# Kernel tuning notes

Hardware: AMD Instinct MI355X
Metric: run time of the kernel (lower is better)

## Reference

```python
import jax, jax.numpy as jnp
import numpy as np

B, P, DIM, H, HKV = 4, 2048, 1024, 16, 8
D = DIM // H  # head_dim = 64


def setup_inputs() -> dict:
    key = jax.random.key(0)
    ks = jax.random.split(key, 5)
    s = lambda fan: 1.0 / np.sqrt(fan)
    return {
        "x": jax.random.normal(ks[0], (B, P, DIM), jnp.float32),
        "Wq": jax.random.normal(ks[1], (DIM, DIM), jnp.float32) * s(DIM),
        "Wk": jax.random.normal(ks[2], (DIM, HKV * D), jnp.float32) * s(DIM),
        "Wv": jax.random.normal(ks[3], (DIM, HKV * D), jnp.float32) * s(DIM),
        "Wp": jax.random.normal(ks[4], (DIM, DIM), jnp.float32) * s(DIM),
        "bp": jnp.zeros((DIM,), jnp.float32),
        "cache": jnp.zeros((HKV,), jnp.float32),  # registered buffer, starts at zero
    }


def _ratios(k, cache):
    # k: [B, HKV, P, D]; torch.norm over dims (2,3) then sum over batch -> [HKV]
    mags = jnp.sqrt((k * k).sum(axis=(2, 3))).sum(axis=0)
    diff = jnp.abs(cache - mags)
    r = jnp.round(diff / diff.sum() * H).astype(jnp.int32)
    # Deterministic repair of rounding so sum(r) == H (original uses random indices)
    r = jax.lax.while_loop(lambda r: r.sum() > H,
                           lambda r: r.at[jnp.argmax(r)].add(-1), r)
    r = jax.lax.while_loop(lambda r: r.sum() < H,
                           lambda r: r.at[jnp.argmin(r)].add(1), r)
    return r


def reference(x, Wq, Wk, Wv, Wp, bp, cache):
    # qkv projections (no bias, per qkv_bias=False)
    q = (x @ Wq).reshape(B, P, H, D).transpose(0, 2, 1, 3) * (D ** -0.5)  # [B,H,P,D]
    k = (x @ Wk).reshape(B, P, HKV, D).transpose(0, 2, 1, 3)              # [B,HKV,P,D]
    v = (x @ Wv).reshape(B, P, HKV, D).transpose(0, 2, 1, 3)

    # dynamic group sizes per kv head (inference path: cache <- magnitudes)
    ratios = jax.lax.stop_gradient(_ratios(k, cache))  # [HKV], sums to H
    # map each query head h to its kv head: group i owns heads [cumsum[i-1], cumsum[i])
    kv_id = jnp.searchsorted(jnp.cumsum(ratios), jnp.arange(H), side='right')

    # gather kv per query head -> identical math to the per-group loop, fully fused
    kf = k[:, kv_id]  # [B,H,P,D]
    vf = v[:, kv_id]
    scores = jnp.einsum('bhqd,bhkd->bhqk', q, kf)   # [B,H,P,P]
    w = jax.nn.softmax(scores, axis=-1)             # attn_drop p=0 -> identity
    out = jnp.einsum('bhqk,bhkd->bhqd', w, vf)
    out = out.transpose(0, 2, 1, 3).reshape(B, P, DIM)
    return out @ Wp + bp  # proj (proj_drop p=0)
```

## Files before the change

kernel.cpp:

```cpp
#include <hip/hip_runtime.h>

typedef __bf16 bf16x8 __attribute__((ext_vector_type(8)));
typedef __bf16 bf16x4 __attribute__((ext_vector_type(4)));
typedef float floatx4 __attribute__((ext_vector_type(4)));

#define BSZ 4
#define SEQ 2048
#define DIM 1024
#define NH 16
#define NKV 8
#define HD 64

#define QSCALE 0.18033688011112042f
#define CSHIFT -14.426950408889634f

#if __has_builtin(__builtin_amdgcn_exp2f)
#define EXP2(x) __builtin_amdgcn_exp2f(x)
#else
#define EXP2(x) exp2f(x)
#endif

#define GLDS16(g, l) __builtin_amdgcn_global_load_lds(                        \
    (const __attribute__((address_space(1))) void*)(g),                       \
    (__attribute__((address_space(3))) void*)(l), 16, 0, 0)

__global__ __launch_bounds__(256) void prep_kernel(
    const float* __restrict__ x,
    const float* __restrict__ Wq, const float* __restrict__ Wk,
    const float* __restrict__ Wv, const float* __restrict__ Wp,
    __bf16* __restrict__ xb, __bf16* __restrict__ Wt, __bf16* __restrict__ Wpt)
{
    __shared__ __bf16 T[64][72];
    const int bid = blockIdx.x;
    const int tid = threadIdx.x;

    if (bid < 2048) {
        size_t i = ((size_t)bid * 256 + tid) * 16;
#pragma unroll
        for (int q = 0; q < 2; ++q) {
            float4 a = *(const float4*)&x[i + q * 8];
            float4 b = *(const float4*)&x[i + q * 8 + 4];
            bf16x8 o;
            o[0] = (__bf16)a.x; o[1] = (__bf16)a.y; o[2] = (__bf16)a.z; o[3] = (__bf16)a.w;
            o[4] = (__bf16)b.x; o[5] = (__bf16)b.y; o[6] = (__bf16)b.z; o[7] = (__bf16)b.w;
            *(bf16x8*)&xb[i + q * 8] = o;
        }
        return;
    }

    const int t  = bid - 2048;
    const int k0 = (t & 15) * 64;
    const int cg = (t >> 4) * 64;

    const float* W; int ldn, cl, orow; __bf16* out;
    if (cg < 1024)      { W = Wq; ldn = 1024; cl = cg;        out = Wt;  orow = cg; }
    else if (cg < 1536) { W = Wk; ldn = 512;  cl = cg - 1024; out = Wt;  orow = cg; }
    else if (cg < 2048) { W = Wv; ldn = 512;  cl = cg - 1536; out = Wt;  orow = cg; }
    else                { W = Wp; ldn = 1024; cl = cg - 2048; out = Wpt; orow = cg - 2048; }

    const int kr = tid >> 2;
    const int cq = (tid & 3) * 16;
#pragma unroll
    for (int j = 0; j < 4; ++j) {
        float4 f = *(const float4*)&W[(size_t)(k0 + kr) * ldn + cl + cq + j * 4];
        T[cq + j * 4 + 0][kr] = (__bf16)f.x;
        T[cq + j * 4 + 1][kr] = (__bf16)f.y;
        T[cq + j * 4 + 2][kr] = (__bf16)f.z;
        T[cq + j * 4 + 3][kr] = (__bf16)f.w;
    }
    __syncthreads();
#pragma unroll
    for (int j = 0; j < 2; ++j) {
        int ch = tid * 2 + j;
        int c = ch >> 3, kc = (ch & 7) * 8;
        *(bf16x8*)&out[(size_t)(orow + c) * 1024 + k0 + kc] = *(bf16x8*)&T[c][kc];
    }
}

#define QSTAGE(bi, kk)                                                        \
    {                                                                         \
        GLDS16(Ag + (kk),             Asb + (bi) * 4096 + wv * 512);          \
        GLDS16(Ag + (kk) + 64 * 1024, Asb + (bi) * 4096 + 2048 + wv * 512);   \
        GLDS16(Bg + (kk),             Bsb + (bi) * 4096 + wv * 512);          \
        GLDS16(Bg + (kk) + 64 * 1024, Bsb + (bi) * 4096 + 2048 + wv * 512);   \
    }

__global__ __launch_bounds__(256) void qkv_gemm(
    const __bf16* __restrict__ xb, const __bf16* __restrict__ Wt,
    __bf16* __restrict__ qw, __bf16* __restrict__ kw, __bf16* __restrict__ vw)
{
    extern __shared__ __align__(16) __bf16 smem[];
    __bf16* Asb = smem;
    __bf16* Bsb = smem + 8192;

    const int m0 = blockIdx.y * 128;
    const int c0 = blockIdx.x * 128;

    const int tid  = threadIdx.x;
    const int lane = tid & 63, wv = tid >> 6;
    const int l16  = lane & 15, quad = lane >> 4;
    const int wr = (wv >> 1) * 64, wc = (wv & 1) * 64;

    const int srow = wv * 16 + (lane >> 2);
    const int skc  = (lane & 3) * 8;
    const __bf16* Ag = xb + (size_t)(m0 + srow) * 1024 + skc;
    const __bf16* Bg = Wt + (size_t)(c0 + srow) * 1024 + skc;

    floatx4 acc[4][4] = {};

    QSTAGE(0, 0);
    __syncthreads();

    for (int t = 0; t < 32; ++t) {
        const int cur = t & 1;
        if (t < 31) QSTAGE(cur ^ 1, (t + 1) * 32);

        bf16x8 af[4], bfr[4];
#pragma unroll
        for (int tt = 0; tt < 4; ++tt) {
            af[tt]  = *(bf16x8*)&Asb[cur * 4096 + (wr + tt * 16 + l16) * 32 + quad * 8];
            bfr[tt] = *(bf16x8*)&Bsb[cur * 4096 + (wc + tt * 16 + l16) * 32 + quad * 8];
        }
#pragma unroll
        for (int mt = 0; mt < 4; ++mt)
#pragma unroll
            for (int nt = 0; nt < 4; ++nt)
                acc[mt][nt] = __builtin_amdgcn_mfma_f32_16x16x32_bf16(
                    af[mt], bfr[nt], acc[mt][nt], 0, 0, 0);
        __syncthreads();
    }

    const int bb = m0 >> 11;
    if (c0 < 1536) {
#pragma unroll
        for (int mt = 0; mt < 4; ++mt) {
#pragma unroll
            for (int nt = 0; nt < 4; ++nt) {
#pragma unroll
                for (int r = 0; r < 4; ++r) {
                    int m = m0 + wr + mt * 16 + quad * 4 + r;
                    int c = c0 + wc + nt * 16 + l16;
                    int p = m & 2047;
                    float val = acc[mt][nt][r];
                    if (c < 1024) {
                        int h = c >> 6, d = c & 63;
                        qw[(((size_t)bb * NH + h) * SEQ + p) * HD + d] = (__bf16)(val * QSCALE);
                    } else {
                        int cc = c - 1024, hh = cc >> 6, d = cc & 63;
                        kw[(((size_t)bb * NKV + hh) * SEQ + p) * HD + d] = (__bf16)val;
                    }
                }
            }
        }
    } else {
        __bf16* T = smem;
#pragma unroll
        for (int mt = 0; mt < 4; ++mt)
#pragma unroll
            for (int nt = 0; nt < 4; ++nt) {
                bf16x4 pv;
#pragma unroll
                for (int r = 0; r < 4; ++r) pv[r] = (__bf16)acc[mt][nt][r];
                *(bf16x4*)&T[(wc + nt * 16 + l16) * 136 + wr + mt * 16 + quad * 4] = pv;
            }
        __syncthreads();

        const int c_l = tid >> 1, half = tid & 1;
        const int cc = c0 - 1536 + c_l, hh = cc >> 6, d = cc & 63;
        const int p0 = (m0 & 2047) + half * 64;
        __bf16* dst = &vw[((size_t)(bb * NKV + hh) * HD + d) * SEQ + p0];
        const __bf16* src = &T[c_l * 136 + half * 64];
#pragma unroll
        for (int i = 0; i < 8; ++i)
            *(bf16x8*)&dst[i * 8] = *(const bf16x8*)&src[i * 8];
    }
}

__global__ __launch_bounds__(256) void ksumsq(const __bf16* __restrict__ kw,
                                              float* __restrict__ partial)
{
    const int blk = blockIdx.x;
    const __bf16* base = kw + (size_t)(blk >> 3) * (SEQ * HD)
                            + (size_t)(blk & 7) * (SEQ * HD / 8);
    const int tid = threadIdx.x;

    float s = 0.f;
#pragma unroll
    for (int i = tid * 8; i < SEQ * HD / 8; i += 256 * 8) {
        bf16x8 vv = *(const bf16x8*)&base[i];
#pragma unroll
        for (int j = 0; j < 8; ++j) { float f = (float)vv[j]; s += f * f; }
    }
#pragma unroll
    for (int off = 1; off < 64; off <<= 1) s += __shfl_xor(s, off, 64);

    __shared__ float red[4];
    if ((tid & 63) == 0) red[tid >> 6] = s;
    __syncthreads();
    if (tid == 0) partial[blk] = red[0] + red[1] + red[2] + red[3];
}

__global__ void ratios_kernel(const float* __restrict__ partial,
                              const float* __restrict__ cache,
                              int* __restrict__ kv_id)
{
    if (threadIdx.x != 0 || blockIdx.x != 0) return;
    float mag[8] = {0.f, 0.f, 0.f, 0.f, 0.f, 0.f, 0.f, 0.f};
    for (int b = 0; b < 4; ++b)
        for (int j = 0; j < 8; ++j) {
            float ss = 0.f;
            for (int sl = 0; sl < 8; ++sl) ss += partial[(b * 8 + j) * 8 + sl];
            mag[j] += sqrtf(ss);
        }
    float diff[8], sum = 0.f;
    for (int j = 0; j < 8; ++j) {
        diff[j] = fabsf(cache[j] - mag[j]);
        sum += diff[j];
    }
    int r[8], s = 0;
    for (int j = 0; j < 8; ++j) {
        r[j] = (int)rintf(diff[j] / sum * 16.0f);
        s += r[j];
    }
    while (s > 16) {
        int jm = 0;
        for (int j = 1; j < 8; ++j) if (r[j] > r[jm]) jm = j;
        r[jm]--; s--;
    }
    while (s < 16) {
        int jm = 0;
        for (int j = 1; j < 8; ++j) if (r[j] < r[jm]) jm = j;
        r[jm]++; s++;
    }
    int cum[8], c = 0;
    for (int j = 0; j < 8; ++j) { c += r[j]; cum[j] = c; }
    for (int h = 0; h < 16; ++h) {
        int j = 0;
        while (j < 7 && cum[j] <= h) j++;
        kv_id[h] = j;
    }
}

__global__ __launch_bounds__(256, 2) void attn_kernel(
    const __bf16* __restrict__ qw, const __bf16* __restrict__ kw,
    const __bf16* __restrict__ vw, const int* __restrict__ kv_id,
    __bf16* __restrict__ attn_out)
{
    __shared__ __align__(16) __bf16 Kt[2][64 * 72];
    __shared__ __align__(16) __bf16 VT[2][64 * 72];

    const int bh = blockIdx.y;
    const int b = bh >> 4, h = bh & 15;
    const int q0 = blockIdx.x * 256;
    const int kv = kv_id[h];

    const __bf16* Kg = kw + ((size_t)(b * NKV + kv) * SEQ) * HD;
    const __bf16* Vg = vw + ((size_t)(b * NKV + kv) * HD) * SEQ;
    const __bf16* Qg = qw + ((size_t)(b * NH + h) * SEQ + q0) * HD;

    const int tid  = threadIdx.x;
    const int lane = tid & 63, wv = tid >> 6;
    const int l16  = lane & 15, quad = lane >> 4;

    bf16x8 qf[4][2];
#pragma unroll
    for (int s = 0; s < 4; ++s) {
        const __bf16* qp = &Qg[(size_t)(64 * wv + 16 * s + l16) * HD];
        qf[s][0] = *(const bf16x8*)&qp[quad * 8];
        qf[s][1] = *(const bf16x8*)&qp[32 + quad * 8];
    }

    bf16x8 vones;
#pragma unroll
    for (int j = 0; j < 8; ++j) vones[j] = (__bf16)1.0f;

    floatx4 o[4][4] = {};
    floatx4 ol[4] = {};

    const int row = tid >> 2, cc = (tid & 3) << 4;
    const __bf16* kp = Kg + (size_t)row * HD + cc;
    const __bf16* vp = Vg + (size_t)row * SEQ + cc;

    bf16x8 rk0 = *(const bf16x8*)kp;
    bf16x8 rk1 = *(const bf16x8*)(kp + 8);
    bf16x8 rv0 = *(const bf16x8*)vp;
    bf16x8 rv1 = *(const bf16x8*)(vp + 8);
    {
        __bf16* kd = &Kt[0][row * 72 + cc];
        *(bf16x8*)kd = rk0; *(bf16x8*)(kd + 8) = rk1;
        __bf16* vd = &VT[0][row * 72 + cc];
        *(bf16x8*)vd = rv0; *(bf16x8*)(vd + 8) = rv1;
    }
    __syncthreads();

    const floatx4 cinit = {CSHIFT, CSHIFT, CSHIFT, CSHIFT};

    for (int kb = 0; kb < 32; ++kb) {
        const int cur = kb & 1;
        const __bf16* Kc = &Kt[cur][0];
        const __bf16* Vc = &VT[cur][0];

        floatx4 sacc[4][4];
#pragma unroll
        for (int s = 0; s < 4; ++s)
#pragma unroll
            for (int t = 0; t < 4; ++t) sacc[s][t] = cinit;
        {
            bf16x8 kf[4];
#pragma unroll
            for (int t = 0; t < 4; ++t)
                kf[t] = *(bf16x8*)&Kc[(16 * t + l16) * 72 + quad * 8];
#pragma unroll
            for (int t = 0; t < 4; ++t)
#pragma unroll
                for (int s = 0; s < 4; ++s)
                    sacc[s][t] = __builtin_amdgcn_mfma_f32_16x16x32_bf16(
                        kf[t], qf[s][0], sacc[s][t], 0, 0, 0);
#pragma unroll
            for (int t = 0; t < 4; ++t)
                kf[t] = *(bf16x8*)&Kc[(16 * t + l16) * 72 + 32 + quad * 8];
#pragma unroll
            for (int t = 0; t < 4; ++t)
#pragma unroll
                for (int s = 0; s < 4; ++s)
                    sacc[s][t] = __builtin_amdgcn_mfma_f32_16x16x32_bf16(
                        kf[t], qf[s][1], sacc[s][t], 0, 0, 0);
        }

        if (kb < 31) {
            const __bf16* kn = kp + (size_t)(kb + 1) * (64 * HD);
            const __bf16* vn = vp + (kb + 1) * 64;
            rk0 = *(const bf16x8*)kn;
            rk1 = *(const bf16x8*)(kn + 8);
            rv0 = *(const bf16x8*)vn;
            rv1 = *(const bf16x8*)(vn + 8);
        }

        bf16x8 a0s[4], a1s[4];
#pragma unroll
        for (int s = 0; s < 4; ++s) {
            bf16x8 a0, a1;
#pragma unroll
            for (int r = 0; r < 4; ++r) {
                float e0 = EXP2(sacc[s][0][r]);
                float e1 = EXP2(sacc[s][1][r]);
                float e2 = EXP2(sacc[s][2][r]);
                float e3 = EXP2(sacc[s][3][r]);
                a0[r] = (__bf16)e0; a0[4 + r] = (__bf16)e1;
                a1[r] = (__bf16)e2; a1[4 + r] = (__bf16)e3;
            }
            a0s[s] = a0; a1s[s] = a1;
        }

#pragma unroll
        for (int s = 0; s < 4; ++s) {
            ol[s] = __builtin_amdgcn_mfma_f32_16x16x32_bf16(a0s[s], vones, ol[s], 0, 0, 0);
            ol[s] = __builtin_amdgcn_mfma_f32_16x16x32_bf16(a1s[s], vones, ol[s], 0, 0, 0);
        }

#pragma unroll
        for (int dt = 0; dt < 4; ++dt) {
            const __bf16* vrow = &Vc[(16 * dt + l16) * 72 + 4 * quad];
            bf16x4 lo0 = *(const bf16x4*)vrow;
            bf16x4 hi0 = *(const bf16x4*)(vrow + 16);
            bf16x8 vb0 = __builtin_shufflevector(lo0, hi0, 0, 1, 2, 3, 4, 5, 6, 7);
#pragma unroll
            for (int s = 0; s < 4; ++s)
                o[s][dt] = __builtin_amdgcn_mfma_f32_16x16x32_bf16(
                    a0s[s], vb0, o[s][dt], 0, 0, 0);
            bf16x4 lo1 = *(const bf16x4*)(vrow + 32);
            bf16x4 hi1 = *(const bf16x4*)(vrow + 48);
            bf16x8 vb1 = __builtin_shufflevector(lo1, hi1, 0, 1, 2, 3, 4, 5, 6, 7);
#pragma unroll
            for (int s = 0; s < 4; ++s)
                o[s][dt] = __builtin_amdgcn_mfma_f32_16x16x32_bf16(
                    a1s[s], vb1, o[s][dt], 0, 0, 0);
        }

        if (kb < 31) {
            __bf16* kd = &Kt[cur ^ 1][row * 72 + cc];
            *(bf16x8*)kd = rk0; *(bf16x8*)(kd + 8) = rk1;
            __bf16* vd = &VT[cur ^ 1][row * 72 + cc];
            *(bf16x8*)vd = rv0; *(bf16x8*)(vd + 8) = rv1;
        }
        __syncthreads();
    }

#pragma unroll
    for (int s = 0; s < 4; ++s) {
#pragma unroll
        for (int r = 0; r < 4; ++r) {
            float inv = 1.f / ol[s][r];
            int p_ = q0 + 64 * wv + 16 * s + quad * 4 + r;
#pragma unroll
            for (int dt = 0; dt < 4; ++dt) {
                int d = 16 * dt + l16;
                attn_out[(((size_t)b * SEQ + p_) * NH + h) * HD + d] = (__bf16)(o[s][dt][r] * inv);
            }
        }
    }
}

#define GSTAGE(bi, kk)                                                        \
    {                                                                         \
        GLDS16(Ag + (kk),             &As[bi][wv * 512]);                     \
        GLDS16(Ag + (kk) + 64 * 1024, &As[bi][2048 + wv * 512]);              \
        GLDS16(Bg + (kk),             &Bs[bi][wv * 512]);                     \
        GLDS16(Bg + (kk) + 64 * 1024, &Bs[bi][2048 + wv * 512]);              \
    }

__global__ __launch_bounds__(256) void proj_gemm(
    const __bf16* __restrict__ A, const __bf16* __restrict__ Wpt,
    const float* __restrict__ bp, float* __restrict__ out)
{
    __shared__ __align__(16) __bf16 As[2][128 * 32];
    __shared__ __align__(16) __bf16 Bs[2][128 * 32];

    const int m0 = blockIdx.y * 128, c0 = blockIdx.x * 128;
    const int tid = threadIdx.x, lane = tid & 63, wv = tid >> 6;
    const int l16 = lane & 15, quad = lane >> 4;
    const int wr = (wv >> 1) * 64, wc = (wv & 1) * 64;

    const int srow = wv * 16 + (lane >> 2);
    const int skc  = (lane & 3) * 8;
    const __bf16* Ag = A   + (size_t)(m0 + srow) * 1024 + skc;
    const __bf16* Bg = Wpt + (size_t)(c0 + srow) * 1024 + skc;

    floatx4 acc[4][4] = {};

    GSTAGE(0, 0);
    __syncthreads();

    for (int t = 0; t < 32; ++t) {
        const int cur = t & 1;
        if (t < 31) GSTAGE(cur ^ 1, (t + 1) * 32);

        bf16x8 af[4], bfr[4];
#pragma unroll
        for (int tt = 0; tt < 4; ++tt) {
            af[tt]  = *(bf16x8*)&As[cur][(wr + tt * 16 + l16) * 32 + quad * 8];
            bfr[tt] = *(bf16x8*)&Bs[cur][(wc + tt * 16 + l16) * 32 + quad * 8];
        }
#pragma unroll
        for (int mt = 0; mt < 4; ++mt)
#pragma unroll
            for (int nt = 0; nt < 4; ++nt)
                acc[mt][nt] = __builtin_amdgcn_mfma_f32_16x16x32_bf16(
                    af[mt], bfr[nt], acc[mt][nt], 0, 0, 0);
        __syncthreads();
    }

#pragma unroll
    for (int nt = 0; nt < 4; ++nt) {
        int c = c0 + wc + nt * 16 + l16;
        float bias = bp[c];
#pragma unroll
        for (int mt = 0; mt < 4; ++mt)
#pragma unroll
            for (int r = 0; r < 4; ++r) {
                int m = m0 + wr + mt * 16 + quad * 4 + r;
                out[(size_t)m * 1024 + c] = acc[mt][nt][r] + bias;
            }
    }
}

extern "C" void kernel_launch(void* const* d_in, const int* in_sizes, int n_in,
                              void* d_out, int out_size, void* d_ws, size_t ws_size,
                              hipStream_t stream)
{
    const float* x     = (const float*)d_in[0];
    const float* Wq    = (const float*)d_in[1];
    const float* Wk    = (const float*)d_in[2];
    const float* Wv    = (const float*)d_in[3];
    const float* Wp    = (const float*)d_in[4];
    const float* bp    = (const float*)d_in[5];
    const float* cache = (const float*)d_in[6];
    float* outp = (float*)d_out;

    __bf16* ws = (__bf16*)d_ws;
    __bf16* qw  = ws;
    __bf16* kw  = qw + (size_t)BSZ * NH * SEQ * HD;
    __bf16* vw  = kw + (size_t)BSZ * NKV * SEQ * HD;
    __bf16* at  = vw + (size_t)BSZ * NKV * SEQ * HD;
    __bf16* xb  = at + (size_t)BSZ * NH * SEQ * HD;
    __bf16* Wt  = xb + (size_t)BSZ * SEQ * DIM;
    __bf16* Wpt = Wt + (size_t)2048 * 1024;
    float* partial = (float*)(Wpt + (size_t)1024 * 1024);
    int*   kv_id   = (int*)(partial + 256);

    prep_kernel<<<2816, 256, 0, stream>>>(x, Wq, Wk, Wv, Wp, xb, Wt, Wpt);
    qkv_gemm<<<dim3(16, 64), 256, 34816, stream>>>(xb, Wt, qw, kw, vw);
    ksumsq<<<256, 256, 0, stream>>>(kw, partial);
    ratios_kernel<<<1, 64, 0, stream>>>(partial, cache, kv_id);
    attn_kernel<<<dim3(8, 64), 256, 0, stream>>>(qw, kw, vw, kv_id, at);
    proj_gemm<<<dim3(8, 64), 256, 0, stream>>>(at, Wpt, bp, outp);
}
```

Before: 265.8 us.

## Fold ratio computation into attention blocks and remap block order for XCD locality

Removes the single-thread ratios_kernel launch. Each attention block now recomputes the head-to-kv-head mapping from the partial sums in thread 0, with the cache values copied into workspace by a small stash kernel. All three GEMM and attention kernels also remap block IDs so that consecutive IDs, which are spread round-robin across the 8 XCDs, land on neighbouring tiles and share L2. This trades one kernel launch for redundant per-block serial work before the main loop, plus a leftover dead duplicate computation block.

```diff
diff --git a/kernel.cpp b/kernel.cpp
--- a/kernel.cpp
+++ b/kernel.cpp
@@ -93,8 +93,10 @@
     __bf16* Asb = smem;
     __bf16* Bsb = smem + 8192;
 
-    const int m0 = blockIdx.y * 128;
-    const int c0 = blockIdx.x * 128;
+    const int id  = blockIdx.x + (blockIdx.y << 4);
+    const int nid = (id & 7) * 128 + (id >> 3);
+    const int m0 = (nid >> 4) * 128;
+    const int c0 = (nid & 15) * 128;
 
     const int tid  = threadIdx.x;
     const int lane = tid & 63, wv = tid >> 6;
@@ -200,67 +202,83 @@
     if (tid == 0) partial[blk] = red[0] + red[1] + red[2] + red[3];
 }
 
-__global__ void ratios_kernel(const float* __restrict__ partial,
-                              const float* __restrict__ cache,
-                              int* __restrict__ kv_id)
-{
-    if (threadIdx.x != 0 || blockIdx.x != 0) return;
-    float mag[8] = {0.f, 0.f, 0.f, 0.f, 0.f, 0.f, 0.f, 0.f};
-    for (int b = 0; b < 4; ++b)
-        for (int j = 0; j < 8; ++j) {
-            float ss = 0.f;
-            for (int sl = 0; sl < 8; ++sl) ss += partial[(b * 8 + j) * 8 + sl];
-            mag[j] += sqrtf(ss);
-        }
-    float diff[8], sum = 0.f;
-    for (int j = 0; j < 8; ++j) {
-        diff[j] = fabsf(cache[j] - mag[j]);
-        sum += diff[j];
-    }
-    int r[8], s = 0;
-    for (int j = 0; j < 8; ++j) {
-        r[j] = (int)rintf(diff[j] / sum * 16.0f);
-        s += r[j];
-    }
-    while (s > 16) {
-        int jm = 0;
-        for (int j = 1; j < 8; ++j) if (r[j] > r[jm]) jm = j;
-        r[jm]--; s--;
-    }
-    while (s < 16) {
-        int jm = 0;
-        for (int j = 1; j < 8; ++j) if (r[j] < r[jm]) jm = j;
-        r[jm]++; s++;
-    }
-    int cum[8], c = 0;
-    for (int j = 0; j < 8; ++j) { c += r[j]; cum[j] = c; }
-    for (int h = 0; h < 16; ++h) {
-        int j = 0;
-        while (j < 7 && cum[j] <= h) j++;
-        kv_id[h] = j;
-    }
-}
-
 __global__ __launch_bounds__(256, 2) void attn_kernel(
     const __bf16* __restrict__ qw, const __bf16* __restrict__ kw,
-    const __bf16* __restrict__ vw, const int* __restrict__ kv_id,
+    const __bf16* __restrict__ vw, const float* __restrict__ partial,
     __bf16* __restrict__ attn_out)
 {
     __shared__ __align__(16) __bf16 Kt[2][64 * 72];
     __shared__ __align__(16) __bf16 VT[2][64 * 72];
-
-    const int bh = blockIdx.y;
+    __shared__ int kv_s;
+
+    const int id  = blockIdx.x + (blockIdx.y << 3);
+    const int nid = (id & 7) * 64 + (id >> 3);
+    const int bh = nid >> 3;
     const int b = bh >> 4, h = bh & 15;
-    const int q0 = blockIdx.x * 256;
-    const int kv = kv_id[h];
+    const int q0 = (nid & 7) * 256;
+
+    const int tid  = threadIdx.x;
+    const int lane = tid & 63, wv = tid >> 6;
+    const int l16  = lane & 15, quad = lane >> 4;
+
+    if (tid == 0) {
+        float mag[8] = {0.f, 0.f, 0.f, 0.f, 0.f, 0.f, 0.f, 0.f};
+        for (int b2 = 0; b2 < 4; ++b2)
+            for (int j = 0; j < 8; ++j) {
+                float ss = 0.f;
+                for (int sl = 0; sl < 8; ++sl) ss += partial[(b2 * 8 + j) * 8 + sl];
+                mag[j] += sqrtf(ss);
+            }
+        float diff[8], sum = 0.f;
+        for (int j = 0; j < 8; ++j) {
+            diff[j] = fabsf(mag[j]);
+            sum += 0.f;
+        }
+        (void)diff; (void)sum;
+        kv_s = 0;
+    }
+    if (tid == 0) {
+        float mag[8] = {0.f, 0.f, 0.f, 0.f, 0.f, 0.f, 0.f, 0.f};
+        for (int b2 = 0; b2 < 4; ++b2)
+            for (int j = 0; j < 8; ++j) {
+                float ss = 0.f;
+                for (int sl = 0; sl < 8; ++sl) ss += partial[(b2 * 8 + j) * 8 + sl];
+                mag[j] += sqrtf(ss);
+            }
+        const float* cache = (const float*)(partial + 256);
+        float diff[8], sum = 0.f;
+        for (int j = 0; j < 8; ++j) {
+            diff[j] = fabsf(cache[j] - mag[j]);
+            sum += diff[j];
+        }
+        int r[8], s = 0;
+        for (int j = 0; j < 8; ++j) {
+            r[j] = (int)rintf(diff[j] / sum * 16.0f);
+            s += r[j];
+        }
+        while (s > 16) {
+            int jm = 0;
+            for (int j = 1; j < 8; ++j) if (r[j] > r[jm]) jm = j;
+            r[jm]--; s--;
+        }
+        while (s < 16) {
+            int jm = 0;
+            for (int j = 1; j < 8; ++j) if (r[j] < r[jm]) jm = j;
+            r[jm]++; s++;
+        }
+        int cum = 0, kvv = 7;
+        for (int j = 0; j < 8; ++j) {
+            cum += r[j];
+            if (h < cum) { kvv = j; break; }
+        }
+        kv_s = kvv;
+    }
+    __syncthreads();
+    const int kv = kv_s;
 
     const __bf16* Kg = kw + ((size_t)(b * NKV + kv) * SEQ) * HD;
     const __bf16* Vg = vw + ((size_t)(b * NKV + kv) * HD) * SEQ;
     const __bf16* Qg = qw + ((size_t)(b * NH + h) * SEQ + q0) * HD;
-
-    const int tid  = threadIdx.x;
-    const int lane = tid & 63, wv = tid >> 6;
-    const int l16  = lane & 15, quad = lane >> 4;
 
     bf16x8 qf[4][2];
 #pragma unroll
@@ -416,7 +434,10 @@
     __shared__ __align__(16) __bf16 As[2][128 * 32];
     __shared__ __align__(16) __bf16 Bs[2][128 * 32];
 
-    const int m0 = blockIdx.y * 128, c0 = blockIdx.x * 128;
+    const int id  = blockIdx.x + (blockIdx.y << 3);
+    const int nid = (id & 7) * 64 + (id >> 3);
+    const int m0 = (nid >> 3) * 128, c0 = (nid & 7) * 128;
+
     const int tid = threadIdx.x, lane = tid & 63, wv = tid >> 6;
     const int l16 = lane & 15, quad = lane >> 4;
     const int wr = (wv >> 1) * 64, wc = (wv & 1) * 64;
@@ -462,6 +483,11 @@
                 out[(size_t)m * 1024 + c] = acc[mt][nt][r] + bias;
             }
     }
+}
+
+__global__ void stash_cache(const float* __restrict__ cache, float* __restrict__ dst)
+{
+    if (threadIdx.x < 8) dst[threadIdx.x] = cache[threadIdx.x];
 }
 
 extern "C" void kernel_launch(void* const* d_in, const int* in_sizes, int n_in,
@@ -486,12 +512,11 @@
     __bf16* Wt  = xb + (size_t)BSZ * SEQ * DIM;
     __bf16* Wpt = Wt + (size_t)2048 * 1024;
     float* partial = (float*)(Wpt + (size_t)1024 * 1024);
-    int*   kv_id   = (int*)(partial + 256);
 
     prep_kernel<<<2816, 256, 0, stream>>>(x, Wq, Wk, Wv, Wp, xb, Wt, Wpt);
+    stash_cache<<<1, 64, 0, stream>>>(cache, partial + 256);
     qkv_gemm<<<dim3(16, 64), 256, 34816, stream>>>(xb, Wt, qw, kw, vw);
     ksumsq<<<256, 256, 0, stream>>>(kw, partial);
-    ratios_kernel<<<1, 64, 0, stream>>>(partial, cache, kv_id);
-    attn_kernel<<<dim3(8, 64), 256, 0, stream>>>(qw, kw, vw, kv_id, at);
+    attn_kernel<<<dim3(8, 64), 256, 0, stream>>>(qw, kw, vw, partial, at);
     proj_gemm<<<dim3(8, 64), 256, 0, stream>>>(at, Wpt, bp, outp);
 }
```

After: 258.8 us. -2.6%, faster.
